# Optimization experiments

Measured on AMD Instinct MI355X. Metric: run time of the kernel, lower is better.

## Reference

```python
import jax, jax.numpy as jnp
import numpy as np

N_NODES = 10000
N_EDGES = 160000
N_FEAT = 512
HEADS = 8
HID = 128
OUT = 16


def setup_inputs() -> dict:
    key = jax.random.key(0)
    ks = jax.random.split(key, 16)
    inp = {
        'node_features': jax.random.normal(ks[0], (N_NODES, N_FEAT), jnp.float32),
        'edge_src': jax.random.randint(ks[1], (N_EDGES,), 0, N_NODES, jnp.int32),
        'edge_dst': jax.random.randint(ks[2], (N_EDGES,), 0, N_NODES, jnp.int32),
        # GAT layer params (scaled randn for numerical sanity)
        'W1': jax.random.normal(ks[3], (HEADS, HID, N_FEAT), jnp.float32) * 0.05,
        'a1': jax.random.normal(ks[4], (HEADS, 2 * HID), jnp.float32) * 0.05,
        'W2': jax.random.normal(ks[5], (HEADS, HID, HID), jnp.float32) * 0.05,
        'a2': jax.random.normal(ks[6], (HEADS, 2 * HID), jnp.float32) * 0.05,
        # MLP: LayerNorm(128) -> Linear(128,64) -> LeakyReLU -> Linear(64,16) -> LeakyReLU -> Linear(16,OUT) -> ReLU
        'ln_g': jnp.ones((HID,), jnp.float32),
        'ln_b': jnp.zeros((HID,), jnp.float32),
        'Wl1': jax.random.normal(ks[7], (64, HID), jnp.float32) * 0.05,
        'bl1': jnp.zeros((64,), jnp.float32),
        'Wl2': jax.random.normal(ks[8], (16, 64), jnp.float32) * 0.05,
        'bl2': jnp.zeros((16,), jnp.float32),
        'Wl3': jax.random.normal(ks[9], (OUT, 16), jnp.float32) * 0.05,
        'bl3': jnp.zeros((OUT,), jnp.float32),
    }
    return inp


def gat_layer(x, src, dst, W, a, n_nodes):
    # per-node, per-head projection: h[n,h,d]
    h = jnp.einsum('hdf,nf->nhd', W, x)
    # split attention vector: e_ij = a[:HID].h_i + a[HID:].h_j
    s_i = jnp.einsum('nhd,hd->nh', h, a[:, :HID])  # score contribution of target i
    s_j = jnp.einsum('nhd,hd->nh', h, a[:, HID:])  # score contribution of neighbor j
    e = jax.nn.leaky_relu(s_i[dst] + s_j[src])     # [E,H], negative_slope=0.01 (torch default)
    # segment softmax over edges grouped by dst
    m = jax.ops.segment_max(e, dst, num_segments=n_nodes)           # [N,H]
    m = jnp.where(jnp.isfinite(m), m, 0.0)
    ex = jnp.exp(e - m[dst])                                        # [E,H]
    denom = jax.ops.segment_sum(ex, dst, num_segments=n_nodes)      # [N,H]
    alpha = ex / jnp.where(denom > 0, denom, 1.0)[dst]              # [E,H]
    # scatter-accumulate weighted neighbor embeddings
    agg = jax.ops.segment_sum(alpha[:, :, None] * h[src], dst, num_segments=n_nodes)  # [N,H,HID]
    # average over heads, ELU (matches 1/attn_heads * attn_sum -> ELU)
    return jax.nn.elu(agg.mean(axis=1))  # [N,HID]


def reference(node_features, edge_src, edge_dst, W1, a1, W2, a2,
              ln_g, ln_b, Wl1, bl1, Wl2, bl2, Wl3, bl3):
    n = node_features.shape[0]
    emb1 = gat_layer(node_features, edge_src, edge_dst, W1, a1, n)
    emb2 = gat_layer(emb1, edge_src, edge_dst, W2, a2, n)
    g = emb2.mean(axis=0)  # [HID] graph embedding
    # MLP head (dropout = identity at inference)
    mu = g.mean()
    var = ((g - mu) ** 2).mean()
    gn = (g - mu) / jnp.sqrt(var + 1e-5) * ln_g + ln_b
    x = jax.nn.leaky_relu(Wl1 @ gn + bl1)
    x = jax.nn.leaky_relu(Wl2 @ x + bl2)
    return jax.nn.relu(Wl3 @ x + bl3)
```

## Files before the change

kernel.cpp:

```cpp
#include <hip/hip_runtime.h>
#include <math.h>

#define N_NODES 10000
#define N_EDGES 160000
#define N_FEAT  512
#define HEADS   8
#define HID     128

typedef __attribute__((ext_vector_type(8))) short bf16x8;
typedef __attribute__((ext_vector_type(4))) float f32x4;
typedef __attribute__((ext_vector_type(2))) float v2f;

__device__ inline unsigned short f2bf_rne(float f) {
  unsigned int u = __float_as_uint(f);
  unsigned int r = u + 0x7fffu + ((u >> 16) & 1u);
  return (unsigned short)(r >> 16);
}
__device__ inline float bf2f(unsigned int b) {
  return __uint_as_float(b << 16);
}

__device__ inline void split_body(const float* __restrict__ in,
                                  unsigned short* __restrict__ hi,
                                  int R, int K8, int idx) {
  int r = idx & 15;
  int t = idx >> 4;
  int kq = t % K8;
  int rb = t / K8;
  int row = rb * 16 + r;
  float v[8] = {0.f, 0.f, 0.f, 0.f, 0.f, 0.f, 0.f, 0.f};
  if (row < R) {
    const float* p = in + (size_t)row * (K8 * 8) + kq * 8;
    float4 a = *(const float4*)p;
    float4 b = *(const float4*)(p + 4);
    v[0] = a.x; v[1] = a.y; v[2] = a.z; v[3] = a.w;
    v[4] = b.x; v[5] = b.y; v[6] = b.z; v[7] = b.w;
  }
  union { unsigned short u[8]; int4 v4; } H;
  #pragma unroll
  for (int e = 0; e < 8; ++e) H.u[e] = f2bf_rne(v[e]);
  *(int4*)&hi[(size_t)idx * 8] = H.v4;
}

__global__ __launch_bounds__(256)
void split_frag2(const float* __restrict__ in1, unsigned short* __restrict__ hi1,
                 int R1, int K81, int total1, int nb1,
                 const float* __restrict__ in2, unsigned short* __restrict__ hi2,
                 int R2, int K82, int total2, int nb2,
                 const float* __restrict__ W2p, unsigned short* __restrict__ hi3,
                 int total3, int nb3,
                 const int* __restrict__ esrc, const int* __restrict__ edst,
                 int* __restrict__ deg, int* __restrict__ slots,
                 int2* __restrict__ ovf, int* __restrict__ cnt, int E,
                 const float* __restrict__ av1, const float* __restrict__ av2,
                 float* __restrict__ wt1, float* __restrict__ wt2) {
  int b = (int)blockIdx.x;
  int tid = threadIdx.x;
  if (b < nb1) {
    int idx = b * 256 + tid;
    if (idx < total1) split_body(in1, hi1, R1, K81, idx);
  } else if (b < nb1 + nb2) {
    int idx = (b - nb1) * 256 + tid;
    if (idx < total2) split_body(in2, hi2, R2, K82, idx);
  } else if (b < nb1 + nb2 + nb3) {
    int idx = (b - nb1 - nb2) * 256 + tid;
    if (idx < total3) split_body(W2p, hi3, HEADS * HID, 16, idx);
  } else {
    int nbE = (E + 255) / 256;
    int eb = b - nb1 - nb2 - nb3;
    if (eb < nbE) {
      int e = eb * 256 + tid;
      if (e < E) {
        int d = edst[e], s = esrc[e];
        int p = atomicAdd(&deg[d], 1);
        if (p < 32) {
          slots[d * 32 + p] = s;
        } else {
          int q = atomicAdd(&cnt[1], 1);
          if (q < E) ovf[q] = make_int2(d, s);
        }
      }
    } else {
      int wb = eb - nbE;
      if (wb < 32) {
        int o = wb * 256 + tid;
        int f = o & 511, ii = (o >> 9) & 1, h = o >> 10;
        const float* Wp = in2 + (size_t)h * HID * N_FEAT + f;
        const float* ap = av1 + h * 2 * HID + ii * HID;
        float c0 = 0.f, c1 = 0.f;
        for (int d = 0; d < HID; d += 2) {
          c0 = fmaf(Wp[(size_t)d * N_FEAT], ap[d], c0);
          c1 = fmaf(Wp[(size_t)(d + 1) * N_FEAT], ap[d + 1], c1);
        }
        wt1[o] = c0 + c1;
      } else {
        int o = (wb - 32) * 256 + tid;
        int f = o & 127, ii = (o >> 7) & 1, h = o >> 8;
        const float* Wp = W2p + (size_t)h * HID * HID + f;
        const float* ap = av2 + h * 2 * HID + ii * HID;
        float c0 = 0.f, c1 = 0.f;
        for (int d = 0; d < HID; d += 2) {
          c0 = fmaf(Wp[(size_t)d * HID], ap[d], c0);
          c1 = fmaf(Wp[(size_t)(d + 1) * HID], ap[d + 1], c1);
        }
        wt2[o] = c0 + c1;
      }
    }
  }
}

__global__ __launch_bounds__(256, 2)
void gemm_score(const unsigned short* __restrict__ Afh,
                const unsigned short* __restrict__ Bfh,
                unsigned short* __restrict__ hb,
                int M, int K, int nbGemm,
                const float* __restrict__ x, const float* __restrict__ wt1,
                float* __restrict__ si, float* __restrict__ sj, int N) {
  int tid = threadIdx.x;
  if ((int)blockIdx.x >= nbGemm) {
    __shared__ float wl[8192];
    #pragma unroll
    for (int k = 0; k < 32; ++k) wl[tid + k * 256] = wt1[tid + k * 256];
    __syncthreads();
    int wv = tid >> 6, lane = tid & 63;
    int rr = lane >> 4, sl = lane & 15;
    int n = ((int)blockIdx.x - nbGemm) * 16 + wv * 4 + rr;
    if (n >= N) return;
    const float* xp = x + (size_t)n * N_FEAT + sl * 4;
    float acc[16];
    #pragma unroll
    for (int t = 0; t < 16; ++t) acc[t] = 0.f;
    #pragma unroll
    for (int k = 0; k < 8; ++k) {
      float4 xv = *(const float4*)(xp + k * 64);
      #pragma unroll
      for (int t = 0; t < 16; ++t) {
        float4 w4 = *(const float4*)&wl[t * 512 + k * 64 + sl * 4];
        acc[t] = fmaf(xv.x, w4.x, fmaf(xv.y, w4.y, fmaf(xv.z, w4.z, fmaf(xv.w, w4.w, acc[t]))));
      }
    }
    #pragma unroll
    for (int o = 1; o <= 8; o <<= 1)
      #pragma unroll
      for (int t = 0; t < 16; ++t) acc[t] += __shfl_xor(acc[t], o);
    float outv = acc[0];
    #pragma unroll
    for (int t = 1; t < 16; ++t) outv = (sl == t) ? acc[t] : outv;
    int h = sl >> 1;
    if (sl & 1) sj[(size_t)h * N + n] = outv;
    else        si[(size_t)h * N + n] = outv;
    return;
  }

  int wave = tid >> 6, lane = tid & 63;
  int r = lane & 15, q = lane >> 4;
  int wr = wave >> 1, wc = wave & 1;

  int blk = blockIdx.x;
  int mtile = blk % 80;
  int head = blk / 80;
  int m0 = mtile * 128;
  int K8 = K >> 3;

  const bf16x8* pA = (const bf16x8*)Afh;
  const bf16x8* pB = (const bf16x8*)Bfh;
  size_t rstep = (size_t)K8 * 16;
  size_t aidx = (size_t)((m0 >> 4) + wr * 4) * rstep + (size_t)q * 16 + r;
  size_t bidx = (size_t)(head * 8 + wc * 4) * rstep + (size_t)q * 16 + r;

  f32x4 acc[4][4] = {};

  for (int k0 = 0; k0 < K; k0 += 128, aidx += 256, bidx += 256) {
    bf16x8 a[16], b[16];
    #pragma unroll
    for (int c = 0; c < 4; ++c)
      #pragma unroll
      for (int i = 0; i < 4; ++i) {
        a[c * 4 + i] = pA[aidx + i * rstep + c * 64];
        b[c * 4 + i] = pB[bidx + i * rstep + c * 64];
      }
    #pragma unroll
    for (int c = 0; c < 4; ++c)
      #pragma unroll
      for (int i = 0; i < 4; ++i)
        #pragma unroll
        for (int j = 0; j < 4; ++j)
          acc[i][j] = __builtin_amdgcn_mfma_f32_16x16x32_bf16(a[c * 4 + i], b[c * 4 + j], acc[i][j], 0, 0, 0);
  }

  #pragma unroll
  for (int i = 0; i < 4; ++i)
    #pragma unroll
    for (int reg = 0; reg < 4; ++reg) {
      int row = m0 + wr * 64 + i * 16 + q * 4 + reg;
      if (row < M) {
        #pragma unroll
        for (int j = 0; j < 4; ++j)
          hb[((size_t)head * M + row) * HID + wc * 64 + j * 16 + r] =
              f2bf_rne(acc[i][j][reg]);
      }
    }
}

__global__ __launch_bounds__(512)
void gat_aggregate9(const unsigned short* __restrict__ hb,
                    const float* __restrict__ si, const float* __restrict__ sj,
                    const int* __restrict__ deg, const int* __restrict__ slots,
                    const int2* __restrict__ ovf, const int* __restrict__ cnt,
                    unsigned short* __restrict__ aggb, int N) {
  __shared__ int2 prs[8][4][32];
  int head = blockIdx.x & 7;
  int wv = threadIdx.x >> 6;
  int lane = threadIdx.x & 63;
  int grp = lane >> 4;
  int sl = lane & 15;
  int n = (blockIdx.x >> 3) * 32 + wv * 4 + grp;
  const unsigned short* hbase = hb + (size_t)head * N * HID;
  const float* sjh = sj + (size_t)head * N;
  bool nv = n < N;
  int dg = 0;
  float s_i = 0.f;
  if (nv) {
    dg = deg[n];
    s_i = si[(size_t)head * N + n];
  }
  int sbase = n * 32;

  int src0 = 0, src1 = 0;
  float sc0 = -INFINITY, sc1 = -INFINITY;
  if (sl < dg) {
    src0 = slots[sbase + sl];
    float t = s_i + sjh[src0];
    sc0 = t > 0.f ? t : 0.01f * t;
  }
  if (16 + sl < dg) {
    src1 = slots[sbase + 16 + sl];
    float t = s_i + sjh[src1];
    sc1 = t > 0.f ? t : 0.01f * t;
  }
  float m = fmaxf(sc0, sc1);
  int oc = 0;
  if (dg > 32) {
    oc = cnt[1];
    if (oc > N_EDGES) oc = N_EDGES;
    for (int e2 = sl; e2 < oc; e2 += 16) {
      int2 pe = ovf[e2];
      if (pe.x == n) {
        float t = s_i + sjh[pe.y];
        t = t > 0.f ? t : 0.01f * t;
        m = fmaxf(m, t);
      }
    }
  }
  #pragma unroll
  for (int o = 1; o <= 8; o <<= 1) m = fmaxf(m, __shfl_xor(m, o));

  float w0 = (sl < dg) ? __expf(sc0 - m) : 0.f;
  float w1 = (16 + sl < dg) ? __expf(sc1 - m) : 0.f;
  float den = w0 + w1;
  if (dg > 32) {
    for (int e2 = sl; e2 < oc; e2 += 16) {
      int2 pe = ovf[e2];
      if (pe.x == n) {
        float t = s_i + sjh[pe.y];
        t = t > 0.f ? t : 0.01f * t;
        den += __expf(t - m);
      }
    }
  }
  #pragma unroll
  for (int o = 1; o <= 8; o <<= 1) den += __shfl_xor(den, o);

  prs[wv][grp][sl] = make_int2(src0, __float_as_int(w0));
  prs[wv][grp][16 + sl] = make_int2(src1, __float_as_int(w1));
  __asm__ volatile("s_waitcnt lgkmcnt(0)" ::: "memory");

  v2f a01 = {0.f, 0.f}, a23 = {0.f, 0.f}, a45 = {0.f, 0.f}, a67 = {0.f, 0.f};
  int dmin = dg < 32 ? dg : 32;
  for (int e0 = 0; e0 < dmin; e0 += 8) {
    int2 p[8];
    #pragma unroll
    for (int u = 0; u < 8; ++u) p[u] = prs[wv][grp][e0 + u];
    int4 pv[8];
    #pragma unroll
    for (int u = 0; u < 8; ++u)
      pv[u] = *(const int4*)&hbase[(size_t)p[u].x * HID + sl * 8];
    #pragma unroll
    for (int u = 0; u < 8; ++u) {
      float w = __int_as_float(p[u].y);
      v2f w2 = {w, w};
      int4 q = pv[u];
      v2f t0 = {bf2f((unsigned)q.x & 0xffffu), __uint_as_float((unsigned)q.x & 0xffff0000u)};
      v2f t1 = {bf2f((unsigned)q.y & 0xffffu), __uint_as_float((unsigned)q.y & 0xffff0000u)};
      v2f t2 = {bf2f((unsigned)q.z & 0xffffu), __uint_as_float((unsigned)q.z & 0xffff0000u)};
      v2f t3 = {bf2f((unsigned)q.w & 0xffffu), __uint_as_float((unsigned)q.w & 0xffff0000u)};
      a01 += w2 * t0;
      a23 += w2 * t1;
      a45 += w2 * t2;
      a67 += w2 * t3;
    }
  }
  if (dg > 32) {
    for (int e2 = 0; e2 < oc; ++e2) {
      int2 pe = ovf[e2];
      if (pe.x != n) continue;
      float t = s_i + sjh[pe.y];
      t = t > 0.f ? t : 0.01f * t;
      float w = __expf(t - m);
      v2f w2 = {w, w};
      int4 q = *(const int4*)&hbase[(size_t)pe.y * HID + sl * 8];
      v2f t0 = {bf2f((unsigned)q.x & 0xffffu), __uint_as_float((unsigned)q.x & 0xffff0000u)};
      v2f t1 = {bf2f((unsigned)q.y & 0xffffu), __uint_as_float((unsigned)q.y & 0xffff0000u)};
      v2f t2 = {bf2f((unsigned)q.z & 0xffffu), __uint_as_float((unsigned)q.z & 0xffff0000u)};
      v2f t3 = {bf2f((unsigned)q.w & 0xffffu), __uint_as_float((unsigned)q.w & 0xffff0000u)};
      a01 += w2 * t0; a23 += w2 * t1; a45 += w2 * t2; a67 += w2 * t3;
    }
  }

  if (nv) {
    float inv = den > 0.f ? 1.0f / den : 0.f;
    union { unsigned short u[8]; int4 v4; } P;
    P.u[0] = f2bf_rne(a01.x * inv); P.u[1] = f2bf_rne(a01.y * inv);
    P.u[2] = f2bf_rne(a23.x * inv); P.u[3] = f2bf_rne(a23.y * inv);
    P.u[4] = f2bf_rne(a45.x * inv); P.u[5] = f2bf_rne(a45.y * inv);
    P.u[6] = f2bf_rne(a67.x * inv); P.u[7] = f2bf_rne(a67.y * inv);
    *(int4*)&aggb[((size_t)head * N + n) * HID + sl * 8] = P.v4;
  }
}

__global__ __launch_bounds__(256)
void headmean_frag2(const unsigned short* __restrict__ aggb,
                    unsigned short* __restrict__ hiA, int N,
                    const float* __restrict__ wt2,
                    float* __restrict__ si, float* __restrict__ sj) {
  __shared__ float wl[2048];
  __shared__ float sred[16][16][17];
  int tid = threadIdx.x;
  #pragma unroll
  for (int k = 0; k < 8; ++k) wl[tid + k * 256] = wt2[tid + k * 256];
  __syncthreads();
  int idx = blockIdx.x * 256 + tid;
  int r = idx & 15;
  int kq = (idx >> 4) & 15;
  int rb = idx >> 8;
  int n = rb * 16 + r;
  float s[8] = {0.f, 0.f, 0.f, 0.f, 0.f, 0.f, 0.f, 0.f};
  if (n < N) {
    #pragma unroll
    for (int hh = 0; hh < HEADS; ++hh) {
      int4 pv = *(const int4*)&aggb[((size_t)hh * N + n) * HID + kq * 8];
      s[0] += bf2f((unsigned)pv.x & 0xffffu);
      s[1] += __uint_as_float((unsigned)pv.x & 0xffff0000u);
      s[2] += bf2f((unsigned)pv.y & 0xffffu);
      s[3] += __uint_as_float((unsigned)pv.y & 0xffff0000u);
      s[4] += bf2f((unsigned)pv.z & 0xffffu);
      s[5] += __uint_as_float((unsigned)pv.z & 0xffff0000u);
      s[6] += bf2f((unsigned)pv.w & 0xffffu);
      s[7] += __uint_as_float((unsigned)pv.w & 0xffff0000u);
    }
  }
  float p[16];
  #pragma unroll
  for (int t = 0; t < 16; ++t) p[t] = 0.f;
  union { unsigned short u[8]; int4 v4; } H;
  #pragma unroll
  for (int e = 0; e < 8; ++e) {
    float v = s[e] * (1.0f / HEADS);
    v = v > 0.f ? v : (__expf(v) - 1.0f);
    #pragma unroll
    for (int t = 0; t < 16; ++t) p[t] = fmaf(v, wl[t * 128 + kq * 8 + e], p[t]);
    H.u[e] = f2bf_rne(v);
  }
  *(int4*)&hiA[(size_t)idx * 8] = H.v4;
  #pragma unroll
  for (int t = 0; t < 16; ++t) sred[kq][r][t] = p[t];
  __syncthreads();
  {
    int rr = tid >> 4, t = tid & 15;
    float sum = 0.f;
    #pragma unroll
    for (int k = 0; k < 16; ++k) sum += sred[k][rr][t];
    int nn = rb * 16 + rr;
    if (nn < N) {
      int h = t >> 1;
      if (t & 1) sj[(size_t)h * N + nn] = sum;
      else       si[(size_t)h * N + nn] = sum;
    }
  }
}

__global__ __launch_bounds__(256)
void headmean_pool(const unsigned short* __restrict__ aggb, float* __restrict__ g,
                   int N) {
  __shared__ float sm[16][128];
  int t = threadIdx.x;
  int nl = t >> 4, dg = t & 15;
  int n = blockIdx.x * 16 + nl;
  float v[8] = {0.f, 0.f, 0.f, 0.f, 0.f, 0.f, 0.f, 0.f};
  if (n < N) {
    #pragma unroll
    for (int hh = 0; hh < HEADS; ++hh) {
      int4 pv = *(const int4*)&aggb[((size_t)hh * N + n) * HID + dg * 8];
      v[0] += bf2f((unsigned)pv.x & 0xffffu);
      v[1] += __uint_as_float((unsigned)pv.x & 0xffff0000u);
      v[2] += bf2f((unsigned)pv.y & 0xffffu);
      v[3] += __uint_as_float((unsigned)pv.y & 0xffff0000u);
      v[4] += bf2f((unsigned)pv.z & 0xffffu);
      v[5] += __uint_as_float((unsigned)pv.z & 0xffff0000u);
      v[6] += bf2f((unsigned)pv.w & 0xffffu);
      v[7] += __uint_as_float((unsigned)pv.w & 0xffff0000u);
    }
    #pragma unroll
    for (int e = 0; e < 8; ++e) {
      float x = v[e] * (1.0f / HEADS);
      v[e] = x > 0.f ? x : (__expf(x) - 1.0f);
    }
  }
  #pragma unroll
  for (int e = 0; e < 8; ++e) sm[nl][dg * 8 + e] = v[e];
  __syncthreads();
  if (t < 128) {
    float s = 0.f;
    #pragma unroll
    for (int nn = 0; nn < 16; ++nn) s += sm[nn][t];
    atomicAdd(&g[t], s);
  }
}

__global__ __launch_bounds__(128)
void mlp_kernel(const float* __restrict__ g, const float* __restrict__ ln_g,
                const float* __restrict__ ln_b, const float* __restrict__ Wl1,
                const float* __restrict__ bl1, const float* __restrict__ Wl2,
                const float* __restrict__ bl2, const float* __restrict__ Wl3,
                const float* __restrict__ bl3, float* __restrict__ out, float invN) {
  __shared__ float red[128];
  __shared__ float gn[128];
  __shared__ float x1[64];
  __shared__ float x2[16];
  int t = threadIdx.x;
  float gg = g[t] * invN;
  red[t] = gg;
  __syncthreads();
  for (int o = 64; o > 0; o >>= 1) {
    if (t < o) red[t] += red[t + o];
    __syncthreads();
  }
  float mu = red[0] * (1.0f / HID);
  __syncthreads();
  float dv = gg - mu;
  red[t] = dv * dv;
  __syncthreads();
  for (int o = 64; o > 0; o >>= 1) {
    if (t < o) red[t] += red[t + o];
    __syncthreads();
  }
  float var = red[0] * (1.0f / HID);
  gn[t] = dv / sqrtf(var + 1e-5f) * ln_g[t] + ln_b[t];
  __syncthreads();
  if (t < 64) {
    float s = bl1[t];
    for (int k = 0; k < 128; ++k) s += Wl1[t * 128 + k] * gn[k];
    x1[t] = s > 0.f ? s : 0.01f * s;
  }
  __syncthreads();
  if (t < 16) {
    float s = bl2[t];
    for (int k = 0; k < 64; ++k) s += Wl2[t * 64 + k] * x1[k];
    x2[t] = s > 0.f ? s : 0.01f * s;
  }
  __syncthreads();
  if (t < 16) {
    float s = bl3[t];
    for (int k = 0; k < 16; ++k) s += Wl3[t * 16 + k] * x2[k];
    out[t] = s > 0.f ? s : 0.f;
  }
}

extern "C" void kernel_launch(void* const* d_in, const int* in_sizes, int n_in,
                              void* d_out, int out_size, void* d_ws, size_t ws_size,
                              hipStream_t stream) {
  const float* x    = (const float*)d_in[0];
  const int*   esrc = (const int*)d_in[1];
  const int*   edst = (const int*)d_in[2];
  const float* W1   = (const float*)d_in[3];
  const float* a1   = (const float*)d_in[4];
  const float* W2   = (const float*)d_in[5];
  const float* a2   = (const float*)d_in[6];
  const float* ln_g = (const float*)d_in[7];
  const float* ln_b = (const float*)d_in[8];
  const float* Wl1  = (const float*)d_in[9];
  const float* bl1  = (const float*)d_in[10];
  const float* Wl2  = (const float*)d_in[11];
  const float* bl2  = (const float*)d_in[12];
  const float* Wl3  = (const float*)d_in[13];
  const float* bl3  = (const float*)d_in[14];
  float* out = (float*)d_out;

  const int RBPAD = 640;

  unsigned short* aggb = (unsigned short*)d_ws;
  float* si   = (float*)(aggb + (size_t)N_NODES * HEADS * HID);
  float* sj   = si + N_NODES * HEADS;
  float* g    = sj + N_NODES * HEADS;
  int*   deg  = (int*)(g + 128);
  int*   cnt  = deg + N_NODES;
  int*   slots= cnt + 4;
  int2*  ovf  = (int2*)(slots + (size_t)N_NODES * 32);
  float* wt1  = (float*)(ovf + N_EDGES);
  float* wt2  = wt1 + 8192;
  unsigned short* Afh  = (unsigned short*)(wt2 + 2048);
  unsigned short* Bfh  = Afh + (size_t)RBPAD * 64 * 128;
  unsigned short* Bfh2 = Bfh + (size_t)1024 * 512;
  unsigned short* hb   = Bfh2 + (size_t)1024 * 128;

  hipMemsetAsync(g, 0, 128 * sizeof(float) + (N_NODES + 4) * sizeof(int), stream);

  int gemmGrid = 80 * HEADS;
  int scoreGrid = (N_NODES + 15) / 16;
  int aggGrid = ((N_NODES + 31) / 32) * 8;

  {
    int totalA = RBPAD * 64 * 16;
    int nbA = (totalA + 255) / 256;
    int totalB = 64 * 64 * 16;
    int nbB = (totalB + 255) / 256;
    int totalB2 = 64 * 16 * 16;
    int nbB2 = (totalB2 + 255) / 256;
    int nbE = (N_EDGES + 255) / 256;
    int nbW = 40;
    split_frag2<<<nbA + nbB + nbB2 + nbE + nbW, 256, 0, stream>>>(
        x, Afh, N_NODES, 64, totalA, nbA,
        W1, Bfh, HEADS * HID, 64, totalB, nbB,
        W2, Bfh2, totalB2, nbB2,
        esrc, edst, deg, slots, ovf, cnt, N_EDGES,
        a1, a2, wt1, wt2);
  }

  gemm_score<<<gemmGrid + scoreGrid, 256, 0, stream>>>(
      Afh, Bfh, hb, N_NODES, N_FEAT, gemmGrid, x, wt1, si, sj, N_NODES);
  gat_aggregate9<<<aggGrid, 512, 0, stream>>>(hb, si, sj, deg, slots, ovf, cnt,
                                              aggb, N_NODES);
  headmean_frag2<<<(N_NODES + 15) / 16, 256, 0, stream>>>(aggb, Afh, N_NODES,
                                                          wt2, si, sj);

  gemm_score<<<gemmGrid, 256, 0, stream>>>(
      Afh, Bfh2, hb, N_NODES, HID, gemmGrid, nullptr, nullptr, nullptr, nullptr, 0);
  gat_aggregate9<<<aggGrid, 512, 0, stream>>>(hb, si, sj, deg, slots, ovf, cnt,
                                              aggb, N_NODES);

  headmean_pool<<<(N_NODES + 15) / 16, 256, 0, stream>>>(aggb, g, N_NODES);
  mlp_kernel<<<1, 128, 0, stream>>>(g, ln_g, ln_b, Wl1, bl1, Wl2, bl2, Wl3, bl3,
                                    out, 1.0f / N_NODES);
}
```

Baseline: 242.7 us.

## Fuse GAT aggregation with head-mean/score and pooling kernels via shared memory

Restructures the aggregation so that each block handles 4 nodes across all 8 heads, with one wave per head. Per-head results are kept in shared memory and the head mean, ELU, next-layer score projection and pooling run inside the same kernel. This drops the bf16 aggb intermediate round-trip through global memory and two kernel launches. In exchange, the block-to-node mapping changes from head-major blocks to node-major blocks, which may hurt L2 locality of the per-head gathered rows. Separate si2/sj2 buffers are added so layer-1 scores are not overwritten while they are still being read.

New measurement: 321.9 us. 32.6% more time.

```diff
diff --git a/kernel.cpp b/kernel.cpp
--- a/kernel.cpp
+++ b/kernel.cpp
@@ -202,28 +202,20 @@
     }
 }
 
-__global__ __launch_bounds__(512)
-void gat_aggregate9(const unsigned short* __restrict__ hb,
-                    const float* __restrict__ si, const float* __restrict__ sj,
-                    const int* __restrict__ deg, const int* __restrict__ slots,
-                    const int2* __restrict__ ovf, const int* __restrict__ cnt,
-                    unsigned short* __restrict__ aggb, int N) {
-  __shared__ int2 prs[8][4][32];
-  int head = blockIdx.x & 7;
-  int wv = threadIdx.x >> 6;
-  int lane = threadIdx.x & 63;
-  int grp = lane >> 4;
-  int sl = lane & 15;
-  int n = (blockIdx.x >> 3) * 32 + wv * 4 + grp;
+__device__ inline void agg_one(const unsigned short* __restrict__ hb,
+                               const float* __restrict__ si,
+                               const float* __restrict__ sj,
+                               const int* __restrict__ deg,
+                               const int* __restrict__ slots,
+                               const int2* __restrict__ ovf,
+                               const int* __restrict__ cnt,
+                               int N, int n, int head, int sl,
+                               int2* __restrict__ prsg,
+                               float* __restrict__ outp) {
   const unsigned short* hbase = hb + (size_t)head * N * HID;
   const float* sjh = sj + (size_t)head * N;
-  bool nv = n < N;
-  int dg = 0;
-  float s_i = 0.f;
-  if (nv) {
-    dg = deg[n];
-    s_i = si[(size_t)head * N + n];
-  }
+  int dg = deg[n];
+  float s_i = si[(size_t)head * N + n];
   int sbase = n * 32;
 
   int src0 = 0, src1 = 0;
@@ -271,8 +263,8 @@
   #pragma unroll
   for (int o = 1; o <= 8; o <<= 1) den += __shfl_xor(den, o);
 
-  prs[wv][grp][sl] = make_int2(src0, __float_as_int(w0));
-  prs[wv][grp][16 + sl] = make_int2(src1, __float_as_int(w1));
+  prsg[sl] = make_int2(src0, __float_as_int(w0));
+  prsg[16 + sl] = make_int2(src1, __float_as_int(w1));
   __asm__ volatile("s_waitcnt lgkmcnt(0)" ::: "memory");
 
   v2f a01 = {0.f, 0.f}, a23 = {0.f, 0.f}, a45 = {0.f, 0.f}, a67 = {0.f, 0.f};
@@ -280,7 +272,7 @@
   for (int e0 = 0; e0 < dmin; e0 += 8) {
     int2 p[8];
     #pragma unroll
-    for (int u = 0; u < 8; ++u) p[u] = prs[wv][grp][e0 + u];
+    for (int u = 0; u < 8; ++u) p[u] = prsg[e0 + u];
     int4 pv[8];
     #pragma unroll
     for (int u = 0; u < 8; ++u)
@@ -317,113 +309,118 @@
     }
   }
 
-  if (nv) {
-    float inv = den > 0.f ? 1.0f / den : 0.f;
-    union { unsigned short u[8]; int4 v4; } P;
-    P.u[0] = f2bf_rne(a01.x * inv); P.u[1] = f2bf_rne(a01.y * inv);
-    P.u[2] = f2bf_rne(a23.x * inv); P.u[3] = f2bf_rne(a23.y * inv);
-    P.u[4] = f2bf_rne(a45.x * inv); P.u[5] = f2bf_rne(a45.y * inv);
-    P.u[6] = f2bf_rne(a67.x * inv); P.u[7] = f2bf_rne(a67.y * inv);
-    *(int4*)&aggb[((size_t)head * N + n) * HID + sl * 8] = P.v4;
-  }
-}
-
-__global__ __launch_bounds__(256)
-void headmean_frag2(const unsigned short* __restrict__ aggb,
-                    unsigned short* __restrict__ hiA, int N,
-                    const float* __restrict__ wt2,
-                    float* __restrict__ si, float* __restrict__ sj) {
-  __shared__ float wl[2048];
-  __shared__ float sred[16][16][17];
+  float inv = den > 0.f ? 1.0f / den : 0.f;
+  outp[0] = bf2f(f2bf_rne(a01.x * inv));
+  outp[1] = bf2f(f2bf_rne(a01.y * inv));
+  outp[2] = bf2f(f2bf_rne(a23.x * inv));
+  outp[3] = bf2f(f2bf_rne(a23.y * inv));
+  outp[4] = bf2f(f2bf_rne(a45.x * inv));
+  outp[5] = bf2f(f2bf_rne(a45.y * inv));
+  outp[6] = bf2f(f2bf_rne(a67.x * inv));
+  outp[7] = bf2f(f2bf_rne(a67.y * inv));
+}
+
+__global__ __launch_bounds__(512)
+void agg_hm(const unsigned short* __restrict__ hb,
+            const float* __restrict__ si, const float* __restrict__ sj,
+            const int* __restrict__ deg, const int* __restrict__ slots,
+            const int2* __restrict__ ovf, const int* __restrict__ cnt,
+            unsigned short* __restrict__ hiA, const float* __restrict__ wt2,
+            float* __restrict__ si2, float* __restrict__ sj2, int N) {
+  __shared__ int2 prs[8][4][32];
+  __shared__ float hm[4][8][128];
+  __shared__ float wl2[2048];
+  __shared__ float sred[16][4][17];
   int tid = threadIdx.x;
   #pragma unroll
-  for (int k = 0; k < 8; ++k) wl[tid + k * 256] = wt2[tid + k * 256];
-  __syncthreads();
-  int idx = blockIdx.x * 256 + tid;
-  int r = idx & 15;
-  int kq = (idx >> 4) & 15;
-  int rb = idx >> 8;
-  int n = rb * 16 + r;
-  float s[8] = {0.f, 0.f, 0.f, 0.f, 0.f, 0.f, 0.f, 0.f};
-  if (n < N) {
-    #pragma unroll
-    for (int hh = 0; hh < HEADS; ++hh) {
-      int4 pv = *(const int4*)&aggb[((size_t)hh * N + n) * HID + kq * 8];
-      s[0] += bf2f((unsigned)pv.x & 0xffffu);
-      s[1] += __uint_as_float((unsigned)pv.x & 0xffff0000u);
-      s[2] += bf2f((unsigned)pv.y & 0xffffu);
-      s[3] += __uint_as_float((unsigned)pv.y & 0xffff0000u);
-      s[4] += bf2f((unsigned)pv.z & 0xffffu);
-      s[5] += __uint_as_float((unsigned)pv.z & 0xffff0000u);
-      s[6] += bf2f((unsigned)pv.w & 0xffffu);
-      s[7] += __uint_as_float((unsigned)pv.w & 0xffff0000u);
-    }
-  }
-  float p[16];
-  #pragma unroll
-  for (int t = 0; t < 16; ++t) p[t] = 0.f;
-  union { unsigned short u[8]; int4 v4; } H;
-  #pragma unroll
-  for (int e = 0; e < 8; ++e) {
-    float v = s[e] * (1.0f / HEADS);
-    v = v > 0.f ? v : (__expf(v) - 1.0f);
-    #pragma unroll
-    for (int t = 0; t < 16; ++t) p[t] = fmaf(v, wl[t * 128 + kq * 8 + e], p[t]);
-    H.u[e] = f2bf_rne(v);
-  }
-  *(int4*)&hiA[(size_t)idx * 8] = H.v4;
-  #pragma unroll
-  for (int t = 0; t < 16; ++t) sred[kq][r][t] = p[t];
-  __syncthreads();
-  {
-    int rr = tid >> 4, t = tid & 15;
+  for (int k = 0; k < 4; ++k) wl2[tid + k * 512] = wt2[tid + k * 512];
+
+  int wv = tid >> 6;
+  int lane = tid & 63;
+  int grp = lane >> 4;
+  int sl = lane & 15;
+  int n = (int)blockIdx.x * 4 + grp;
+  if (n < N)
+    agg_one(hb, si, sj, deg, slots, ovf, cnt, N, n, wv, sl,
+            &prs[wv][grp][0], &hm[grp][wv][sl * 8]);
+  __syncthreads();
+
+  if (tid < 64) {
+    int d = tid >> 4, kq = tid & 15;
+    int nn = (int)blockIdx.x * 4 + d;
+    float s[8] = {0.f, 0.f, 0.f, 0.f, 0.f, 0.f, 0.f, 0.f};
+    #pragma unroll
+    for (int h = 0; h < HEADS; ++h)
+      #pragma unroll
+      for (int e = 0; e < 8; ++e) s[e] += hm[d][h][kq * 8 + e];
+    float p[16];
+    #pragma unroll
+    for (int t = 0; t < 16; ++t) p[t] = 0.f;
+    union { unsigned short u[8]; int4 v4; } H;
+    #pragma unroll
+    for (int e = 0; e < 8; ++e) {
+      float v = s[e] * (1.0f / HEADS);
+      v = v > 0.f ? v : (__expf(v) - 1.0f);
+      #pragma unroll
+      for (int t = 0; t < 16; ++t) p[t] = fmaf(v, wl2[t * 128 + kq * 8 + e], p[t]);
+      H.u[e] = f2bf_rne(v);
+    }
+    if (nn < N) {
+      size_t idx = ((size_t)(nn >> 4) * 16 + kq) * 16 + (nn & 15);
+      *(int4*)&hiA[idx * 8] = H.v4;
+    }
+    #pragma unroll
+    for (int t = 0; t < 16; ++t) sred[kq][d][t] = p[t];
+  }
+  __syncthreads();
+  if (tid < 64) {
+    int d = tid >> 4, t = tid & 15;
     float sum = 0.f;
     #pragma unroll
-    for (int k = 0; k < 16; ++k) sum += sred[k][rr][t];
-    int nn = rb * 16 + rr;
+    for (int k = 0; k < 16; ++k) sum += sred[k][d][t];
+    int nn = (int)blockIdx.x * 4 + d;
     if (nn < N) {
       int h = t >> 1;
-      if (t & 1) sj[(size_t)h * N + nn] = sum;
-      else       si[(size_t)h * N + nn] = sum;
-    }
-  }
-}
-
-__global__ __launch_bounds__(256)
-void headmean_pool(const unsigned short* __restrict__ aggb, float* __restrict__ g,
-                   int N) {
-  __shared__ float sm[16][128];
-  int t = threadIdx.x;
-  int nl = t >> 4, dg = t & 15;
-  int n = blockIdx.x * 16 + nl;
-  float v[8] = {0.f, 0.f, 0.f, 0.f, 0.f, 0.f, 0.f, 0.f};
-  if (n < N) {
-    #pragma unroll
-    for (int hh = 0; hh < HEADS; ++hh) {
-      int4 pv = *(const int4*)&aggb[((size_t)hh * N + n) * HID + dg * 8];
-      v[0] += bf2f((unsigned)pv.x & 0xffffu);
-      v[1] += __uint_as_float((unsigned)pv.x & 0xffff0000u);
-      v[2] += bf2f((unsigned)pv.y & 0xffffu);
-      v[3] += __uint_as_float((unsigned)pv.y & 0xffff0000u);
-      v[4] += bf2f((unsigned)pv.z & 0xffffu);
-      v[5] += __uint_as_float((unsigned)pv.z & 0xffff0000u);
-      v[6] += bf2f((unsigned)pv.w & 0xffffu);
-      v[7] += __uint_as_float((unsigned)pv.w & 0xffff0000u);
-    }
-    #pragma unroll
-    for (int e = 0; e < 8; ++e) {
-      float x = v[e] * (1.0f / HEADS);
-      v[e] = x > 0.f ? x : (__expf(x) - 1.0f);
-    }
-  }
-  #pragma unroll
-  for (int e = 0; e < 8; ++e) sm[nl][dg * 8 + e] = v[e];
-  __syncthreads();
-  if (t < 128) {
+      if (t & 1) sj2[(size_t)h * N + nn] = sum;
+      else       si2[(size_t)h * N + nn] = sum;
+    }
+  }
+}
+
+__global__ __launch_bounds__(512)
+void agg_pool(const unsigned short* __restrict__ hb,
+              const float* __restrict__ si, const float* __restrict__ sj,
+              const int* __restrict__ deg, const int* __restrict__ slots,
+              const int2* __restrict__ ovf, const int* __restrict__ cnt,
+              float* __restrict__ g, int N) {
+  __shared__ int2 prs[8][4][32];
+  __shared__ float hm[4][8][128];
+  __shared__ float pb[4][128];
+  int tid = threadIdx.x;
+  int wv = tid >> 6;
+  int lane = tid & 63;
+  int grp = lane >> 4;
+  int sl = lane & 15;
+  int n = (int)blockIdx.x * 4 + grp;
+  if (n < N)
+    agg_one(hb, si, sj, deg, slots, ovf, cnt, N, n, wv, sl,
+            &prs[wv][grp][0], &hm[grp][wv][sl * 8]);
+  __syncthreads();
+
+  {
+    int d = tid >> 7, dim = tid & 127;
+    int nn = (int)blockIdx.x * 4 + d;
     float s = 0.f;
     #pragma unroll
-    for (int nn = 0; nn < 16; ++nn) s += sm[nn][t];
-    atomicAdd(&g[t], s);
+    for (int h = 0; h < HEADS; ++h) s += hm[d][h][dim];
+    float v = s * (1.0f / HEADS);
+    v = v > 0.f ? v : (__expf(v) - 1.0f);
+    pb[d][dim] = (nn < N) ? v : 0.f;
+  }
+  __syncthreads();
+  if (tid < 128) {
+    float s = pb[0][tid] + pb[1][tid] + pb[2][tid] + pb[3][tid];
+    atomicAdd(&g[tid], s);
   }
 }
 
@@ -498,8 +495,9 @@
 
   const int RBPAD = 640;
 
-  unsigned short* aggb = (unsigned short*)d_ws;
-  float* si   = (float*)(aggb + (size_t)N_NODES * HEADS * HID);
+  float* si2  = (float*)d_ws;
+  float* sj2  = si2 + N_NODES * HEADS;
+  float* si   = (float*)((unsigned short*)d_ws + (size_t)N_NODES * HEADS * HID);
   float* sj   = si + N_NODES * HEADS;
   float* g    = sj + N_NODES * HEADS;
   int*   deg  = (int*)(g + 128);
@@ -517,7 +515,7 @@
 
   int gemmGrid = 80 * HEADS;
   int scoreGrid = (N_NODES + 15) / 16;
-  int aggGrid = ((N_NODES + 31) / 32) * 8;
+  int aggGrid = (N_NODES + 3) / 4;
 
   {
     int totalA = RBPAD * 64 * 16;
@@ -538,17 +536,16 @@
 
   gemm_score<<<gemmGrid + scoreGrid, 256, 0, stream>>>(
       Afh, Bfh, hb, N_NODES, N_FEAT, gemmGrid, x, wt1, si, sj, N_NODES);
-  gat_aggregate9<<<aggGrid, 512, 0, stream>>>(hb, si, sj, deg, slots, ovf, cnt,
-                                              aggb, N_NODES);
-  headmean_frag2<<<(N_NODES + 15) / 16, 256, 0, stream>>>(aggb, Afh, N_NODES,
-                                                          wt2, si, sj);
+
+  agg_hm<<<aggGrid, 512, 0, stream>>>(hb, si, sj, deg, slots, ovf, cnt,
+                                      Afh, wt2, si2, sj2, N_NODES);
 
   gemm_score<<<gemmGrid, 256, 0, stream>>>(
       Afh, Bfh2, hb, N_NODES, HID, gemmGrid, nullptr, nullptr, nullptr, nullptr, 0);
-  gat_aggregate9<<<aggGrid, 512, 0, stream>>>(hb, si, sj, deg, slots, ovf, cnt,
-                                              aggb, N_NODES);
-
-  headmean_pool<<<(N_NODES + 15) / 16, 256, 0, stream>>>(aggb, g, N_NODES);
+
+  agg_pool<<<aggGrid, 512, 0, stream>>>(hb, si2, sj2, deg, slots, ovf, cnt,
+                                        g, N_NODES);
+
   mlp_kernel<<<1, 128, 0, stream>>>(g, ln_g, ln_b, Wl1, bl1, Wl2, bl2, Wl3, bl3,
                                     out, 1.0f / N_NODES);
 }
```
